# Kernel tuning notes

Measured on AMD Instinct MI355X. Metric: run time of the kernel, lower is better.

Reference implementation:

```python
import jax, jax.numpy as jnp
import numpy as np

B = 64                      # batch_size: number of candidate elements
N_PER = 100_000             # observations per candidate
DATA = B * N_PER            # data_size
EPS = 1e-6
INV_ROOT_2PI = 1.0 / np.sqrt(2.0 * np.pi)

def _deg2dist(deg):
    # chord distance on unit sphere subtended by angle deg
    return 2.0 * np.sin(np.radians(deg) / 2.0)

THRESH_DEG = 1.0
THRESH_S2_MIN = np.float32(_deg2dist(10.0 / 3600.0) ** 2)
THRESH_S2_MAX = np.float32(_deg2dist(THRESH_DEG) ** 2)
LOG_THRESH_S2_RANGE = np.float32(np.log(THRESH_S2_MAX / THRESH_S2_MIN))


def setup_inputs() -> dict:
    key = jax.random.key(0)
    k1, k2, k3, k4, k5 = jax.random.split(key, 5)
    u_obs = jax.random.normal(k1, (DATA, 3), dtype=jnp.float32)
    u_obs = u_obs / jnp.linalg.norm(u_obs, axis=-1, keepdims=True)   # unit directions
    # predicted directions = observed + small perturbation so some obs fall inside threshold
    u_pred = u_obs + 0.01 * jax.random.normal(k2, (DATA, 3), dtype=jnp.float32)
    u_pred = u_pred / jnp.linalg.norm(u_pred, axis=-1, keepdims=True)
    mag_obs = 18.0 + jax.random.normal(k3, (DATA,), dtype=jnp.float32)
    R_elt = 0.001 + 0.004 * jax.random.uniform(k4, (B,), dtype=jnp.float32)  # resolution param
    thresh_s2_ = jax.random.uniform(k5, (B,), dtype=jnp.float32)             # trainable, in [0,1]
    seg_ids = jnp.repeat(jnp.arange(B, dtype=jnp.int32), N_PER)              # ragged row_lengths -> segment ids
    return {"u_pred": u_pred, "R_elt": R_elt, "u_obs": u_obs,
            "mag_obs": mag_obs, "thresh_s2_": thresh_s2_, "seg_ids": seg_ids}


def reference(u_pred, R_elt, u_obs, mag_obs, thresh_s2_, seg_ids):
    # threshold transform (get_thresh_s2)
    thresh_s2_elt = THRESH_S2_MIN * jnp.exp(thresh_s2_ * LOG_THRESH_S2_RANGE)    # [B]
    thresh_all = thresh_s2_elt[seg_ids]                                          # [DATA]

    # calc_dist: squared chord distance + threshold mask
    du = u_pred - u_obs
    s2 = jnp.sum(du * du, axis=-1)                                               # [DATA]
    is_close = s2 < thresh_all                                                   # bool [DATA]
    mask = is_close.astype(s2.dtype)
    v = s2 / thresh_all                                                          # in [0,1] on close obs

    # cond_pdf_dist: exponential-family pdf conditional on a hit (q_miss = 1)
    lam_elt = 0.5 * thresh_s2_elt / (R_elt * R_elt)                              # [B]
    lam = lam_elt[seg_ids]                                                       # [DATA]
    log_q_hit = -lam * v + jnp.log(lam) - jnp.log1p(-jnp.exp(-lam))              # log(e^{-lam v} lam / (1 - e^{-lam}))

    # mag_standardize: per-candidate mean/std over close observations -> z-score
    n_close = jax.ops.segment_sum(mask, seg_ids, num_segments=B, indices_are_sorted=True)
    n_safe = jnp.maximum(n_close, 1.0)
    sum_m = jax.ops.segment_sum(mask * mag_obs, seg_ids, num_segments=B, indices_are_sorted=True)
    sum_m2 = jax.ops.segment_sum(mask * mag_obs * mag_obs, seg_ids, num_segments=B, indices_are_sorted=True)
    mu = sum_m / n_safe                                                          # [B]
    var = jnp.maximum(sum_m2 / n_safe - mu * mu, EPS)
    sigma_hat = jnp.sqrt(var)                                                    # [B]

    z = (mag_obs - mu[seg_ids]) / sigma_hat[seg_ids]                             # [DATA]
    log_p_mag = jnp.log(INV_ROOT_2PI / sigma_hat[seg_ids]) - 0.5 * z * z

    # per-candidate score: segment-sum of log conditional densities on close obs
    score = jax.ops.segment_sum(mask * (log_q_hit + log_p_mag), seg_ids,
                                num_segments=B, indices_are_sorted=True)         # [B]
    return score
```

## Files before the change

### kernel.cpp

```cpp
#include <hip/hip_runtime.h>
#include <math.h>


#define BLOCK 256
#define BPS   25

__global__ __launch_bounds__(BLOCK) void ts_main_kernel(
    const float* __restrict__ u_pred,
    const float* __restrict__ u_obs,
    const float* __restrict__ mag,
    const float* __restrict__ thresh_raw,
    float* __restrict__ acc,
    int n_per, float ts_min, float log_range)
{
    const int seg   = blockIdx.x / BPS;
    const int cid   = blockIdx.x % BPS;
    const int chunk = n_per / BPS;
    const long long base0 = (long long)seg * n_per + (long long)cid * chunk;

    const float thresh = ts_min * expf(thresh_raw[seg] * log_range);

    float cnt = 0.f, sm = 0.f, sm2 = 0.f, ss2 = 0.f;

    const int ngroups = chunk >> 2;
    for (int g = threadIdx.x; g < ngroups; g += BLOCK) {
        const long long base = base0 + ((long long)g << 2);
        const float4* up = reinterpret_cast<const float4*>(u_pred + base * 3);
        const float4* uo = reinterpret_cast<const float4*>(u_obs  + base * 3);
        const float4  a0 = up[0], a1 = up[1], a2 = up[2];
        const float4  b0 = uo[0], b1 = uo[1], b2 = uo[2];
        const float4  mg = *reinterpret_cast<const float4*>(mag + base);

        float dx, dy, dz, s2;

        dx = a0.x - b0.x; dy = a0.y - b0.y; dz = a0.z - b0.z;
        s2 = dx*dx + dy*dy + dz*dz;
        if (s2 < thresh) { cnt += 1.f; sm += mg.x; sm2 += mg.x*mg.x; ss2 += s2; }

        dx = a0.w - b0.w; dy = a1.x - b1.x; dz = a1.y - b1.y;
        s2 = dx*dx + dy*dy + dz*dz;
        if (s2 < thresh) { cnt += 1.f; sm += mg.y; sm2 += mg.y*mg.y; ss2 += s2; }

        dx = a1.z - b1.z; dy = a1.w - b1.w; dz = a2.x - b2.x;
        s2 = dx*dx + dy*dy + dz*dz;
        if (s2 < thresh) { cnt += 1.f; sm += mg.z; sm2 += mg.z*mg.z; ss2 += s2; }

        dx = a2.y - b2.y; dy = a2.z - b2.z; dz = a2.w - b2.w;
        s2 = dx*dx + dy*dy + dz*dz;
        if (s2 < thresh) { cnt += 1.f; sm += mg.w; sm2 += mg.w*mg.w; ss2 += s2; }
    }

    for (int off = 32; off > 0; off >>= 1) {
        cnt += __shfl_down(cnt, off);
        sm  += __shfl_down(sm,  off);
        sm2 += __shfl_down(sm2, off);
        ss2 += __shfl_down(ss2, off);
    }

    __shared__ float red[4][BLOCK / 64];
    const int wave = threadIdx.x >> 6;
    const int lane = threadIdx.x & 63;
    if (lane == 0) {
        red[0][wave] = cnt; red[1][wave] = sm;
        red[2][wave] = sm2; red[3][wave] = ss2;
    }
    __syncthreads();
    if (threadIdx.x == 0) {
        float t0 = 0.f, t1 = 0.f, t2 = 0.f, t3 = 0.f;
        #pragma unroll
        for (int w = 0; w < BLOCK / 64; ++w) {
            t0 += red[0][w]; t1 += red[1][w]; t2 += red[2][w]; t3 += red[3][w];
        }
        atomicAdd(&acc[seg * 4 + 0], t0);
        atomicAdd(&acc[seg * 4 + 1], t1);
        atomicAdd(&acc[seg * 4 + 2], t2);
        atomicAdd(&acc[seg * 4 + 3], t3);
    }
}

__global__ void ts_final_kernel(
    const float* __restrict__ acc,
    const float* __restrict__ R_elt,
    const float* __restrict__ thresh_raw,
    float* __restrict__ out,
    int Bn, float ts_min, float log_range)
{
    const int b = blockIdx.x * blockDim.x + threadIdx.x;
    if (b >= Bn) return;

    const float n   = acc[b * 4 + 0];
    const float sm  = acc[b * 4 + 1];
    const float sm2 = acc[b * 4 + 2];
    const float ss2 = acc[b * 4 + 3];

    float score = 0.f;
    if (n > 0.f) {
        const float thresh = ts_min * expf(thresh_raw[b] * log_range);
        const float R   = R_elt[b];
        const float lam = 0.5f * thresh / (R * R);
        const float C   = logf(lam) - logf(-expm1f(-lam));

        const float ssd     = sm2 - sm * (sm / n);
        const float var_raw = ssd / n;
        const float var     = fmaxf(var_raw, 1e-6f);
        const float sigma   = sqrtf(var);
        const float log_inv_root_2pi = -0.9189385332046727f;

        score = -lam * (ss2 / thresh)
              + n * C
              + n * (log_inv_root_2pi - logf(sigma))
              - 0.5f * (ssd / var);
    }
    out[b] = score;
}

extern "C" void kernel_launch(void* const* d_in, const int* in_sizes, int n_in,
                              void* d_out, int out_size, void* d_ws, size_t ws_size,
                              hipStream_t stream) {
    const float* u_pred     = (const float*)d_in[0];
    const float* R_elt      = (const float*)d_in[1];
    const float* u_obs      = (const float*)d_in[2];
    const float* mag_obs    = (const float*)d_in[3];
    const float* thresh_raw = (const float*)d_in[4];

    const int B    = in_sizes[1];
    const int DATA = in_sizes[3];
    const int n_per = DATA / B;

    float* acc = (float*)d_ws;
    float* out = (float*)d_out;

    const double rad_min = M_PI / 180.0 * (10.0 / 3600.0);
    const double rad_max = M_PI / 180.0 * 1.0;
    const float ts_min = (float)((2.0 * sin(rad_min / 2.0)) * (2.0 * sin(rad_min / 2.0)));
    const float ts_max = (float)((2.0 * sin(rad_max / 2.0)) * (2.0 * sin(rad_max / 2.0)));
    const float log_range = logf(ts_max / ts_min);

    hipMemsetAsync(acc, 0, (size_t)B * 4 * sizeof(float), stream);

    ts_main_kernel<<<B * BPS, BLOCK, 0, stream>>>(
        u_pred, u_obs, mag_obs, thresh_raw, acc, n_per, ts_min, log_range);

    ts_final_kernel<<<1, 64, 0, stream>>>(
        acc, R_elt, thresh_raw, out, B, ts_min, log_range);
}
```

Measured before the change: 42.92 us.

## Coalesce loads per wave via LDS transpose with register prefetch and wave-level atomics

Each wave now handles 256-observation tiles. It loads the interleaved xyz arrays with fully coalesced float4 accesses, squares the differences and writes them to shared memory. It then reads them back regrouped so each lane can form per-observation sums. The next tile is prefetched into registers while the current one is computed, and the grid drops to 16 blocks per segment. The block-level shared reduction is replaced by per-wave atomics that are skipped when the count is zero, which adds LDS traffic and more atomics in exchange for better coalescing and latency hiding.

```diff
diff --git a/kernel.cpp b/kernel.cpp
--- a/kernel.cpp
+++ b/kernel.cpp
@@ -3,9 +3,13 @@
 
 
 #define BLOCK 256
-#define BPS   25
+#define WAVES 4
+#define SEG_BLOCKS 16
+#define WPSEG (SEG_BLOCKS * WAVES)
+#define TILE_OBS 256
+#define TILE_FLT 768
 
-__global__ __launch_bounds__(BLOCK) void ts_main_kernel(
+__global__ __launch_bounds__(BLOCK, 4) void ts_main_kernel(
     const float* __restrict__ u_pred,
     const float* __restrict__ u_obs,
     const float* __restrict__ mag,
@@ -13,41 +17,89 @@
     float* __restrict__ acc,
     int n_per, float ts_min, float log_range)
 {
-    const int seg   = blockIdx.x / BPS;
-    const int cid   = blockIdx.x % BPS;
-    const int chunk = n_per / BPS;
-    const long long base0 = (long long)seg * n_per + (long long)cid * chunk;
+    __shared__ float d2s[WAVES][TILE_FLT];
+
+    const int seg  = blockIdx.x / SEG_BLOCKS;
+    const int cid  = blockIdx.x % SEG_BLOCKS;
+    const int widx = threadIdx.x >> 6;
+    const int lane = threadIdx.x & 63;
+    const int wv   = cid * WAVES + widx;
+
+    const long long segO = (long long)seg * n_per;
+    const float* predB = u_pred + segO * 3;
+    const float* obsB  = u_obs  + segO * 3;
+    const float* magB  = mag + segO;
 
     const float thresh = ts_min * expf(thresh_raw[seg] * log_range);
 
+    const int nt    = (n_per + TILE_OBS - 1) / TILE_OBS;
+    const int maxFo = n_per * 3 - 4;
+    const int maxMo = n_per - 4;
+
+    float* wlds = d2s[widx];
+
     float cnt = 0.f, sm = 0.f, sm2 = 0.f, ss2 = 0.f;
 
-    const int ngroups = chunk >> 2;
-    for (int g = threadIdx.x; g < ngroups; g += BLOCK) {
-        const long long base = base0 + ((long long)g << 2);
-        const float4* up = reinterpret_cast<const float4*>(u_pred + base * 3);
-        const float4* uo = reinterpret_cast<const float4*>(u_obs  + base * 3);
-        const float4  a0 = up[0], a1 = up[1], a2 = up[2];
-        const float4  b0 = uo[0], b1 = uo[1], b2 = uo[2];
-        const float4  mg = *reinterpret_cast<const float4*>(mag + base);
+    float4 P0, P1, P2, O0, O1, O2, M;
 
-        float dx, dy, dz, s2;
+    auto loadTile = [&](int t, float4& p0, float4& p1, float4& p2,
+                        float4& o0, float4& o1, float4& o2, float4& m) {
+        const int fb = t * TILE_FLT + lane * 4;
+        const int f0 = min(fb,       maxFo);
+        const int f1 = min(fb + 256, maxFo);
+        const int f2 = min(fb + 512, maxFo);
+        p0 = *(const float4*)(predB + f0);
+        p1 = *(const float4*)(predB + f1);
+        p2 = *(const float4*)(predB + f2);
+        o0 = *(const float4*)(obsB + f0);
+        o1 = *(const float4*)(obsB + f1);
+        o2 = *(const float4*)(obsB + f2);
+        const int mo = min(t * TILE_OBS + lane * 4, maxMo);
+        m = *(const float4*)(magB + mo);
+    };
 
-        dx = a0.x - b0.x; dy = a0.y - b0.y; dz = a0.z - b0.z;
-        s2 = dx*dx + dy*dy + dz*dz;
-        if (s2 < thresh) { cnt += 1.f; sm += mg.x; sm2 += mg.x*mg.x; ss2 += s2; }
+    int t = wv;
+    if (t < nt) loadTile(t, P0, P1, P2, O0, O1, O2, M);
 
-        dx = a0.w - b0.w; dy = a1.x - b1.x; dz = a1.y - b1.y;
-        s2 = dx*dx + dy*dy + dz*dz;
-        if (s2 < thresh) { cnt += 1.f; sm += mg.y; sm2 += mg.y*mg.y; ss2 += s2; }
+    while (t < nt) {
+        const int tn = t + WPSEG;
+        float4 Q0, Q1, Q2, R0, R1, R2, N;
+        const bool pf = tn < nt;
+        if (pf) loadTile(tn, Q0, Q1, Q2, R0, R1, R2, N);
+        __builtin_amdgcn_sched_barrier(0);
 
-        dx = a1.z - b1.z; dy = a1.w - b1.w; dz = a2.x - b2.x;
-        s2 = dx*dx + dy*dy + dz*dz;
-        if (s2 < thresh) { cnt += 1.f; sm += mg.z; sm2 += mg.z*mg.z; ss2 += s2; }
+        float4 a, b, c;
+        { float d;
+          d = P0.x-O0.x; a.x = d*d;  d = P0.y-O0.y; a.y = d*d;
+          d = P0.z-O0.z; a.z = d*d;  d = P0.w-O0.w; a.w = d*d;
+          d = P1.x-O1.x; b.x = d*d;  d = P1.y-O1.y; b.y = d*d;
+          d = P1.z-O1.z; b.z = d*d;  d = P1.w-O1.w; b.w = d*d;
+          d = P2.x-O2.x; c.x = d*d;  d = P2.y-O2.y; c.y = d*d;
+          d = P2.z-O2.z; c.z = d*d;  d = P2.w-O2.w; c.w = d*d; }
 
-        dx = a2.y - b2.y; dy = a2.z - b2.z; dz = a2.w - b2.w;
-        s2 = dx*dx + dy*dy + dz*dz;
-        if (s2 < thresh) { cnt += 1.f; sm += mg.w; sm2 += mg.w*mg.w; ss2 += s2; }
+        *(float4*)(wlds + 4 * lane)        = a;
+        *(float4*)(wlds + 256 + 4 * lane)  = b;
+        *(float4*)(wlds + 512 + 4 * lane)  = c;
+        const float4 r0 = *(const float4*)(wlds + 12 * lane);
+        const float4 r1 = *(const float4*)(wlds + 12 * lane + 4);
+        const float4 r2 = *(const float4*)(wlds + 12 * lane + 8);
+
+        const float s2v[4] = { r0.x + r0.y + r0.z,
+                               r0.w + r1.x + r1.y,
+                               r1.z + r1.w + r2.x,
+                               r2.y + r2.z + r2.w };
+        const float mv[4] = { M.x, M.y, M.z, M.w };
+        const int jb = t * TILE_OBS + 4 * lane;
+
+        #pragma unroll
+        for (int i = 0; i < 4; ++i) {
+            if ((jb + i) < n_per && s2v[i] < thresh) {
+                cnt += 1.f; sm += mv[i]; sm2 += mv[i] * mv[i]; ss2 += s2v[i];
+            }
+        }
+
+        t = tn;
+        if (pf) { P0 = Q0; P1 = Q1; P2 = Q2; O0 = R0; O1 = R1; O2 = R2; M = N; }
     }
 
     for (int off = 32; off > 0; off >>= 1) {
@@ -56,25 +108,11 @@
         sm2 += __shfl_down(sm2, off);
         ss2 += __shfl_down(ss2, off);
     }
-
-    __shared__ float red[4][BLOCK / 64];
-    const int wave = threadIdx.x >> 6;
-    const int lane = threadIdx.x & 63;
-    if (lane == 0) {
-        red[0][wave] = cnt; red[1][wave] = sm;
-        red[2][wave] = sm2; red[3][wave] = ss2;
-    }
-    __syncthreads();
-    if (threadIdx.x == 0) {
-        float t0 = 0.f, t1 = 0.f, t2 = 0.f, t3 = 0.f;
-        #pragma unroll
-        for (int w = 0; w < BLOCK / 64; ++w) {
-            t0 += red[0][w]; t1 += red[1][w]; t2 += red[2][w]; t3 += red[3][w];
-        }
-        atomicAdd(&acc[seg * 4 + 0], t0);
-        atomicAdd(&acc[seg * 4 + 1], t1);
-        atomicAdd(&acc[seg * 4 + 2], t2);
-        atomicAdd(&acc[seg * 4 + 3], t3);
+    if (lane == 0 && cnt != 0.f) {
+        atomicAdd(&acc[seg * 4 + 0], cnt);
+        atomicAdd(&acc[seg * 4 + 1], sm);
+        atomicAdd(&acc[seg * 4 + 2], sm2);
+        atomicAdd(&acc[seg * 4 + 3], ss2);
     }
 }
 
@@ -123,8 +161,8 @@
     const float* mag_obs    = (const float*)d_in[3];
     const float* thresh_raw = (const float*)d_in[4];
 
-    const int B    = in_sizes[1];
-    const int DATA = in_sizes[3];
+    const int B     = in_sizes[1];
+    const int DATA  = in_sizes[3];
     const int n_per = DATA / B;
 
     float* acc = (float*)d_ws;
@@ -138,7 +176,7 @@
 
     hipMemsetAsync(acc, 0, (size_t)B * 4 * sizeof(float), stream);
 
-    ts_main_kernel<<<B * BPS, BLOCK, 0, stream>>>(
+    ts_main_kernel<<<B * SEG_BLOCKS, BLOCK, 0, stream>>>(
         u_pred, u_obs, mag_obs, thresh_raw, acc, n_per, ts_min, log_range);
 
     ts_final_kernel<<<1, 64, 0, stream>>>(
```

New measurement: 56.25 us. +31.1%, slower.
